# Optimization experiments

Hardware: AMD Instinct MI355X
Metric: run time of the kernel (lower is better)

Reference implementation:

```python
import jax, jax.numpy as jnp
import numpy as np

TEMPERATURE = 0.1
SIGMA = 1.0
NUM_CLASSES = 4
INF = 1e8
EPS = 1e-12


def _l2_normalize(x):
    n = jnp.sqrt(jnp.sum(x * x, axis=-1, keepdims=True))
    return x / jnp.maximum(n, EPS)


def _rbf_kernel(y, gamma):
    # y: [M, P] -> [M, M] exp(-gamma * ||yi - yj||^2)
    sq = jnp.sum(y * y, axis=-1)
    d2 = sq[:, None] + sq[None, :] - 2.0 * (y @ y.T)
    d2 = jnp.maximum(d2, 0.0)
    return jnp.exp(-gamma * d2)


def setup_inputs() -> dict:
    key = jax.random.key(0)
    k1, k2, k3, k4 = jax.random.split(key, 4)
    N, D = 2048, 512
    return {
        "z_i": jax.random.normal(k1, (N, D), dtype=jnp.float32),
        "z_j": jax.random.normal(k2, (N, D), dtype=jnp.float32),
        "labels": jax.random.randint(k3, (N,), 0, NUM_CLASSES, dtype=jnp.int64),
        "z_pos": jax.random.uniform(k4, (N, 1), dtype=jnp.float32),
    }


def reference(z_i, z_j, labels, z_pos):
    N = z_i.shape[0]
    zi = _l2_normalize(z_i)
    zj = _l2_normalize(z_j)

    eye_n = jnp.eye(N, dtype=zi.dtype)
    sim_zii = (zi @ zi.T) / TEMPERATURE - INF * eye_n
    sim_zjj = (zj @ zj.T) / TEMPERATURE - INF * eye_n
    sim_zij = (zi @ zj.T) / TEMPERATURE

    # label agreement mask over the 2N x 2N augmented batch
    labs = jax.nn.one_hot(labels, NUM_CLASSES, dtype=jnp.float32)
    L = jnp.concatenate([labs, labs], axis=0)          # [2N, C]
    eye_2n = jnp.eye(2 * N, dtype=jnp.float32)
    mask = (L @ L.T) * (1.0 - eye_2n)

    # RBF kernel weights over positional labels (detached in original)
    all_pos = jnp.tile(z_pos.reshape(N, -1), (2, 1))   # [2N, P]
    gamma = 1.0 / (2.0 * SIGMA ** 2)
    weights = _rbf_kernel(all_pos, gamma) * (1.0 - eye_2n)

    final_weights = weights * mask
    # NB: torch broadcasting divides column j by rowsum[j]; matrix is symmetric
    final_weights = final_weights / final_weights.sum(axis=1)

    top = jnp.concatenate([sim_zii, sim_zij], axis=1)
    bot = jnp.concatenate([sim_zij.T, sim_zjj], axis=1)
    sim_Z = jnp.concatenate([top, bot], axis=0)        # [2N, 2N]

    log_sim_Z = jax.nn.log_softmax(sim_Z, axis=1)
    loss = (-1.0 / N) * jnp.sum(log_sim_Z * final_weights)
    return loss
```

## Files before the change

kernel.cpp:

```cpp
#include <hip/hip_runtime.h>
#include <hip/hip_bf16.h>

#define D 512
#define INV_T 10.0f
#define INF_VAL 1e8f

#define TILE 256
#define BK 32
#define KSTEPS (D / BK)
#define NGT 16
#define NGB (NGT * NGT)
#define TTB 64
#define NCHUNK 64

typedef short bf16x8 __attribute__((ext_vector_type(8)));
typedef float f32x4 __attribute__((ext_vector_type(4)));

typedef __attribute__((address_space(3))) unsigned int lds_uint;
typedef __attribute__((address_space(1))) unsigned int gbl_uint;

__device__ __forceinline__ void async_copy16(const ushort* gsrc, ushort* ldst) {
  __builtin_amdgcn_global_load_lds((const gbl_uint*)gsrc, (lds_uint*)ldst, 16, 0, 0);
}

__device__ inline float wave_reduce_sum(float v) {
#pragma unroll
  for (int off = 32; off > 0; off >>= 1) v += __shfl_xor(v, off);
  return v;
}

__device__ __forceinline__ ushort f2bf(float x) {
  __hip_bfloat16 h = __float2bfloat16(x);
  return *reinterpret_cast<ushort*>(&h);
}

__global__ __launch_bounds__(256) void k_prep(const float* __restrict__ zi,
                                              const float* __restrict__ zj,
                                              ushort* __restrict__ zb,
                                              const int* __restrict__ labels,
                                              const float* __restrict__ zpos,
                                              float* __restrict__ sinv, int N) {
  int b = blockIdx.x;
  if (b < 1024) {
    int wv = threadIdx.x >> 6, lane = threadIdx.x & 63;
    int row = b * 4 + wv;
    const float* src = (row < N) ? (zi + (size_t)row * D) : (zj + (size_t)(row - N) * D);
    const float4* s4 = reinterpret_cast<const float4*>(src);
    float4 v0 = s4[lane];
    float4 v1 = s4[lane + 64];
    float ss = 0.f;
    ss = fmaf(v0.x, v0.x, ss); ss = fmaf(v0.y, v0.y, ss);
    ss = fmaf(v0.z, v0.z, ss); ss = fmaf(v0.w, v0.w, ss);
    ss = fmaf(v1.x, v1.x, ss); ss = fmaf(v1.y, v1.y, ss);
    ss = fmaf(v1.z, v1.z, ss); ss = fmaf(v1.w, v1.w, ss);
    ss = wave_reduce_sum(ss);
    float sc = 1.0f / fmaxf(sqrtf(ss), 1e-12f);
    ushort4 o0 = {f2bf(v0.x * sc), f2bf(v0.y * sc), f2bf(v0.z * sc), f2bf(v0.w * sc)};
    ushort4 o1 = {f2bf(v1.x * sc), f2bf(v1.y * sc), f2bf(v1.z * sc), f2bf(v1.w * sc)};
    ushort4* dst = reinterpret_cast<ushort4*>(zb + (size_t)row * D);
    dst[lane] = o0;
    dst[lane + 64] = o1;
  } else {
    __shared__ float scratch[4];
    int j = b - 1024;
    int lj = labels[j];
    float pj = zpos[j];
    float s = 0.f;
    for (int i = threadIdx.x; i < N; i += 256) {
      if (labels[i] == lj) {
        float d = zpos[i] - pj;
        s += __expf(-0.5f * d * d);
      }
    }
    s = wave_reduce_sum(s);
    int lane = threadIdx.x & 63, wv = threadIdx.x >> 6;
    if (lane == 0) scratch[wv] = s;
    __syncthreads();
    if (threadIdx.x == 0) {
      float t = scratch[0] + scratch[1] + scratch[2] + scratch[3];
      sinv[j] = 1.0f / (2.0f * t - 1.0f);
    }
  }
}

__global__ __launch_bounds__(512, 2) void k_main(
    const ushort* __restrict__ zb, const int* __restrict__ labels,
    const float* __restrict__ zpos, const float* __restrict__ sinv,
    float* __restrict__ tt,
    float* __restrict__ s_ws, float* __restrict__ c_ws, int N) {
  const int tid = threadIdx.x;
  const int bid = blockIdx.x;
  const int twoN = 2 * N;

  if (bid < TTB) {
    int i = bid * 32 + (tid >> 4);
    int part = tid & 15;
    int li = labels[i];
    float pi = zpos[i];
    int seg = N >> 4;
    float s = 0.f;
    for (int j = part * seg; j < (part + 1) * seg; ++j) {
      if (labels[j] == li) {
        float d = zpos[j] - pi;
        s += __expf(-0.5f * d * d) * sinv[j];
      }
    }
    s += __shfl_xor(s, 1); s += __shfl_xor(s, 2);
    s += __shfl_xor(s, 4); s += __shfl_xor(s, 8);
    if (part == 0) tt[i] = s;
    return;
  }

  __shared__ __align__(16) ushort As[2][TILE * BK];
  __shared__ __align__(16) ushort Bs[2][TILE * BK];

  const int lane = tid & 63;
  const int wv = tid >> 6;
  const int wr = wv >> 2;
  const int wc = wv & 3;
  const int colq = lane & 15;
  const int laneg = lane >> 4;

  int b = bid - TTB;
  int L = (b & 7) * 32 + (b >> 3);
  const int rt = L >> 4;
  const int ct = L & 15;
  const int rowBase = rt * TILE;
  const int colBase = ct * TILE;

  const int srow = lane >> 2;
  const int sslot = (lane & 3) ^ ((lane >> 3) & 3);

  f32x4 acc[8][4] = {};

#define STAGE(buf, kt)                                                        \
  {                                                                           \
    _Pragma("unroll")                                                         \
    for (int q = 0; q < 2; ++q) {                                             \
      int r0 = wv * 32 + q * 16;                                              \
      async_copy16(zb + (size_t)(rowBase + r0 + srow) * D + (kt) * BK +       \
                       sslot * 8,                                             \
                   As[buf] + r0 * BK);                                        \
      async_copy16(zb + (size_t)(colBase + r0 + srow) * D + (kt) * BK +       \
                       sslot * 8,                                             \
                   Bs[buf] + r0 * BK);                                        \
    }                                                                         \
  }

  STAGE(0, 0);
  __syncthreads();

  int cur = 0;
#pragma unroll
  for (int kt = 0; kt < KSTEPS; ++kt) {
    if (kt + 1 < KSTEPS) STAGE(cur ^ 1, kt + 1);

    const char* Ab = reinterpret_cast<const char*>(As[cur]);
    const char* Bb = reinterpret_cast<const char*>(Bs[cur]);
    bf16x8 a[8], bf[4];
#pragma unroll
    for (int rf = 0; rf < 8; ++rf) {
      int r = wr * 128 + rf * 16 + colq;
      a[rf] = *reinterpret_cast<const bf16x8*>(
          Ab + r * 64 + ((laneg ^ ((r >> 1) & 3)) << 4));
    }
#pragma unroll
    for (int cf = 0; cf < 4; ++cf) {
      int c = wc * 64 + cf * 16 + colq;
      bf[cf] = *reinterpret_cast<const bf16x8*>(
          Bb + c * 64 + ((laneg ^ ((c >> 1) & 3)) << 4));
    }
#pragma unroll
    for (int rf = 0; rf < 8; ++rf)
#pragma unroll
      for (int cf = 0; cf < 4; ++cf)
        acc[rf][cf] = __builtin_amdgcn_mfma_f32_16x16x32_bf16(a[rf], bf[cf], acc[rf][cf], 0, 0, 0);

    if (kt + 1 < KSTEPS) {
      __syncthreads();
      cur ^= 1;
    }
  }
#undef STAGE

  const int wRowBase = rowBase + wr * 128;
  const int wColBase = colBase + wc * 64;
  const int rmodBase = (wRowBase >= N) ? wRowBase - N : wRowBase;
  const int cmodBase = (wColBase >= N) ? wColBase - N : wColBase;

  int lc[4]; float pc[4], si[4];
#pragma unroll
  for (int cf = 0; cf < 4; ++cf) {
    int jc = cmodBase + cf * 16 + colq;
    lc[cf] = labels[jc];
    pc[cf] = zpos[jc];
    si[cf] = sinv[jc];
  }
  const int m = ct * 4 + wc;

#pragma unroll
  for (int rf = 0; rf < 8; ++rf) {
    float rpos[4]; int rlab[4];
#pragma unroll
    for (int rg = 0; rg < 4; ++rg) {
      int r = rmodBase + rf * 16 + laneg * 4 + rg;
      rpos[rg] = zpos[r];
      rlab[rg] = labels[r];
    }
    float s_p[4] = {0.f, 0.f, 0.f, 0.f};
    float c_p[4] = {0.f, 0.f, 0.f, 0.f};
#pragma unroll
    for (int cf = 0; cf < 4; ++cf) {
      int col = wColBase + cf * 16 + colq;
#pragma unroll
      for (int rg = 0; rg < 4; ++rg) {
        int row = wRowBase + rf * 16 + laneg * 4 + rg;
        float sim = acc[rf][cf][rg] * INV_T;
        bool dg = (row == col);
        if (dg) sim = -INF_VAL;
        s_p[rg] += __expf(sim - 10.f);
        if (rlab[rg] == lc[cf] && !dg) {
          float d = rpos[rg] - pc[cf];
          c_p[rg] = fmaf(__expf(-0.5f * d * d) * si[cf], sim, c_p[rg]);
        }
      }
    }
#pragma unroll
    for (int rg = 0; rg < 4; ++rg) {
#pragma unroll
      for (int off = 1; off < 16; off <<= 1) {
        s_p[rg] += __shfl_xor(s_p[rg], off);
        c_p[rg] += __shfl_xor(c_p[rg], off);
      }
    }
    if (colq == 0) {
#pragma unroll
      for (int rg = 0; rg < 4; ++rg) {
        int row = wRowBase + rf * 16 + laneg * 4 + rg;
        s_ws[(size_t)m * twoN + row] = s_p[rg];
        c_ws[(size_t)m * twoN + row] = c_p[rg];
      }
    }
  }
}

__global__ __launch_bounds__(256) void k_combine(const float* __restrict__ s_ws,
                                                 const float* __restrict__ c_ws,
                                                 const float* __restrict__ sinv,
                                                 const float* __restrict__ tt,
                                                 float* __restrict__ bsum, int N) {
  __shared__ float sS[4][64], sC[4][64];
  int b = blockIdx.x, t = threadIdx.x;
  int r = t & 63, g = t >> 6;
  int twoN = 2 * N;
  int a = b * 64 + r;
  float s = 0.f, c = 0.f;
  for (int k = 0; k < NCHUNK / 4; ++k) {
    int m = g * (NCHUNK / 4) + k;
    s += s_ws[(size_t)m * twoN + a];
    c += c_ws[(size_t)m * twoN + a];
  }
  sS[g][r] = s;
  sC[g][r] = c;
  __syncthreads();
  if (t < 64) {
    float st = sS[0][t] + sS[1][t] + sS[2][t] + sS[3][t];
    float ct = sC[0][t] + sC[1][t] + sC[2][t] + sC[3][t];
    int aa = b * 64 + t;
    int ir = (aa >= N) ? aa - N : aa;
    float lse = 10.f + logf(st);
    float wsum = 2.f * tt[ir] - sinv[ir];
    float p = ct - wsum * lse;
    p = wave_reduce_sum(p);
    if (t == 0) bsum[b] = p;
  }
}

__global__ __launch_bounds__(64) void k_final(const float* __restrict__ bsum,
                                              float* __restrict__ out, int N) {
  float s = bsum[threadIdx.x];
  s = wave_reduce_sum(s);
  if (threadIdx.x == 0) out[0] = (-1.0f / (float)N) * s;
}

extern "C" void kernel_launch(void* const* d_in, const int* in_sizes, int n_in,
                              void* d_out, int out_size, void* d_ws, size_t ws_size,
                              hipStream_t stream) {
  (void)n_in; (void)out_size; (void)ws_size;
  const float* zi = (const float*)d_in[0];
  const float* zj = (const float*)d_in[1];
  const int* labels = (const int*)d_in[2];
  const float* zpos = (const float*)d_in[3];
  float* out = (float*)d_out;

  const int N = in_sizes[2];
  const int twoN = 2 * N;

  char* wsb = (char*)d_ws;
  ushort* zb = (ushort*)wsb;
  float* sinv = (float*)(wsb + (size_t)twoN * D * 2);
  float* tt = sinv + N;
  float* s_ws = tt + N;
  float* c_ws = s_ws + (size_t)NCHUNK * twoN;
  float* bsum = c_ws + (size_t)NCHUNK * twoN;

  k_prep<<<1024 + 2048, 256, 0, stream>>>(zi, zj, zb, labels, zpos, sinv, N);
  k_main<<<TTB + NGB, 512, 0, stream>>>(zb, labels, zpos, sinv, tt, s_ws, c_ws, N);
  k_combine<<<twoN / 64, 256, 0, stream>>>(s_ws, c_ws, sinv, tt, bsum, N);
  k_final<<<1, 64, 0, stream>>>(bsum, out, N);
}
```

Measured before the change: 70.75 us.

## Shrink GEMM tiles to 128x128 with 256-thread blocks and restructure epilogue

The fused similarity GEMM now uses 128x128 output tiles computed by four waves in 256-thread blocks, instead of 256x256 tiles with 512 threads. That gives 1024 tiles rather than 256, spreading work more evenly across CUs and allowing more resident blocks per CU. The epilogue now keeps all 16 row partials in registers, packs row labels into a bitfield, loads each column's metadata once, and reduces once at the end. The label-weight blocks move to the end of the grid and handle 16 rows each. Smaller tiles reuse each loaded operand less, so L2 and global load traffic rises.

```diff
diff --git a/kernel.cpp b/kernel.cpp
--- a/kernel.cpp
+++ b/kernel.cpp
@@ -5,12 +5,12 @@
 #define INV_T 10.0f
 #define INF_VAL 1e8f
 
-#define TILE 256
+#define BM 128
 #define BK 32
 #define KSTEPS (D / BK)
-#define NGT 16
-#define NGB (NGT * NGT)
-#define TTB 64
+#define NTB 32
+#define NGB (NTB * NTB)
+#define TTBLK 128
 #define NCHUNK 64
 
 typedef short bf16x8 __attribute__((ext_vector_type(8)));
@@ -83,7 +83,7 @@
   }
 }
 
-__global__ __launch_bounds__(512, 2) void k_main(
+__global__ __launch_bounds__(256, 4) void k_gemm(
     const ushort* __restrict__ zb, const int* __restrict__ labels,
     const float* __restrict__ zpos, const float* __restrict__ sinv,
     float* __restrict__ tt,
@@ -92,8 +92,8 @@
   const int bid = blockIdx.x;
   const int twoN = 2 * N;
 
-  if (bid < TTB) {
-    int i = bid * 32 + (tid >> 4);
+  if (bid >= NGB) {
+    int i = (bid - NGB) * 16 + (tid >> 4);
     int part = tid & 15;
     int li = labels[i];
     float pi = zpos[i];
@@ -111,27 +111,26 @@
     return;
   }
 
-  __shared__ __align__(16) ushort As[2][TILE * BK];
-  __shared__ __align__(16) ushort Bs[2][TILE * BK];
+  __shared__ __align__(16) ushort As[2][BM * BK];
+  __shared__ __align__(16) ushort Bs[2][BM * BK];
 
   const int lane = tid & 63;
   const int wv = tid >> 6;
-  const int wr = wv >> 2;
-  const int wc = wv & 3;
+  const int wr = wv >> 1;
+  const int wc = wv & 1;
   const int colq = lane & 15;
   const int laneg = lane >> 4;
 
-  int b = bid - TTB;
-  int L = (b & 7) * 32 + (b >> 3);
-  const int rt = L >> 4;
-  const int ct = L & 15;
-  const int rowBase = rt * TILE;
-  const int colBase = ct * TILE;
+  const int L = (bid & 7) * 128 + (bid >> 3);
+  const int rt = L >> 5;
+  const int ct = L & 31;
+  const int rowBase = rt * BM;
+  const int colBase = ct * BM;
 
   const int srow = lane >> 2;
   const int sslot = (lane & 3) ^ ((lane >> 3) & 3);
 
-  f32x4 acc[8][4] = {};
+  f32x4 acc[4][4] = {};
 
 #define STAGE(buf, kt)                                                        \
   {                                                                           \
@@ -157,24 +156,24 @@
 
     const char* Ab = reinterpret_cast<const char*>(As[cur]);
     const char* Bb = reinterpret_cast<const char*>(Bs[cur]);
-    bf16x8 a[8], bf[4];
-#pragma unroll
-    for (int rf = 0; rf < 8; ++rf) {
-      int r = wr * 128 + rf * 16 + colq;
+    bf16x8 a[4], b[4];
+#pragma unroll
+    for (int rf = 0; rf < 4; ++rf) {
+      int r = wr * 64 + rf * 16 + colq;
       a[rf] = *reinterpret_cast<const bf16x8*>(
           Ab + r * 64 + ((laneg ^ ((r >> 1) & 3)) << 4));
     }
 #pragma unroll
     for (int cf = 0; cf < 4; ++cf) {
       int c = wc * 64 + cf * 16 + colq;
-      bf[cf] = *reinterpret_cast<const bf16x8*>(
+      b[cf] = *reinterpret_cast<const bf16x8*>(
           Bb + c * 64 + ((laneg ^ ((c >> 1) & 3)) << 4));
     }
 #pragma unroll
-    for (int rf = 0; rf < 8; ++rf)
+    for (int rf = 0; rf < 4; ++rf)
 #pragma unroll
       for (int cf = 0; cf < 4; ++cf)
-        acc[rf][cf] = __builtin_amdgcn_mfma_f32_16x16x32_bf16(a[rf], bf[cf], acc[rf][cf], 0, 0, 0);
+        acc[rf][cf] = __builtin_amdgcn_mfma_f32_16x16x32_bf16(a[rf], b[cf], acc[rf][cf], 0, 0, 0);
 
     if (kt + 1 < KSTEPS) {
       __syncthreads();
@@ -183,64 +182,71 @@
   }
 #undef STAGE
 
-  const int wRowBase = rowBase + wr * 128;
+  const int wRowBase = rowBase + wr * 64;
   const int wColBase = colBase + wc * 64;
   const int rmodBase = (wRowBase >= N) ? wRowBase - N : wRowBase;
   const int cmodBase = (wColBase >= N) ? wColBase - N : wColBase;
 
-  int lc[4]; float pc[4], si[4];
+  float rpos[16];
+  unsigned rlab = 0;
+#pragma unroll
+  for (int rf = 0; rf < 4; ++rf)
+#pragma unroll
+    for (int rg = 0; rg < 4; ++rg) {
+      int idx = rf * 4 + rg;
+      int r = rmodBase + rf * 16 + laneg * 4 + rg;
+      rpos[idx] = zpos[r];
+      rlab |= ((unsigned)labels[r] & 3u) << (idx * 2);
+    }
+
+  float s_p[16], c_p[16];
+#pragma unroll
+  for (int i = 0; i < 16; ++i) { s_p[i] = 0.f; c_p[i] = 0.f; }
+
 #pragma unroll
   for (int cf = 0; cf < 4; ++cf) {
     int jc = cmodBase + cf * 16 + colq;
-    lc[cf] = labels[jc];
-    pc[cf] = zpos[jc];
-    si[cf] = sinv[jc];
-  }
-  const int m = ct * 4 + wc;
-
-#pragma unroll
-  for (int rf = 0; rf < 8; ++rf) {
-    float rpos[4]; int rlab[4];
-#pragma unroll
-    for (int rg = 0; rg < 4; ++rg) {
-      int r = rmodBase + rf * 16 + laneg * 4 + rg;
-      rpos[rg] = zpos[r];
-      rlab[rg] = labels[r];
-    }
-    float s_p[4] = {0.f, 0.f, 0.f, 0.f};
-    float c_p[4] = {0.f, 0.f, 0.f, 0.f};
-#pragma unroll
-    for (int cf = 0; cf < 4; ++cf) {
-      int col = wColBase + cf * 16 + colq;
+    int lc = labels[jc];
+    float pc = zpos[jc];
+    float si = sinv[jc];
+    int col = wColBase + cf * 16 + colq;
+#pragma unroll
+    for (int rf = 0; rf < 4; ++rf)
 #pragma unroll
       for (int rg = 0; rg < 4; ++rg) {
+        int idx = rf * 4 + rg;
         int row = wRowBase + rf * 16 + laneg * 4 + rg;
         float sim = acc[rf][cf][rg] * INV_T;
         bool dg = (row == col);
         if (dg) sim = -INF_VAL;
-        s_p[rg] += __expf(sim - 10.f);
-        if (rlab[rg] == lc[cf] && !dg) {
-          float d = rpos[rg] - pc[cf];
-          c_p[rg] = fmaf(__expf(-0.5f * d * d) * si[cf], sim, c_p[rg]);
+        s_p[idx] += __expf(sim - 10.f);
+        int lr = (int)((rlab >> (idx * 2)) & 3u);
+        if (lr == lc && !dg) {
+          float d = rpos[idx] - pc;
+          c_p[idx] = fmaf(__expf(-0.5f * d * d) * si, sim, c_p[idx]);
         }
       }
-    }
-#pragma unroll
-    for (int rg = 0; rg < 4; ++rg) {
-#pragma unroll
-      for (int off = 1; off < 16; off <<= 1) {
-        s_p[rg] += __shfl_xor(s_p[rg], off);
-        c_p[rg] += __shfl_xor(c_p[rg], off);
+  }
+
+#pragma unroll
+  for (int idx = 0; idx < 16; ++idx) {
+#pragma unroll
+    for (int off = 1; off < 16; off <<= 1) {
+      s_p[idx] += __shfl_xor(s_p[idx], off);
+      c_p[idx] += __shfl_xor(c_p[idx], off);
+    }
+  }
+  if (colq == 0) {
+    int m = ct * 2 + wc;
+#pragma unroll
+    for (int rf = 0; rf < 4; ++rf)
+#pragma unroll
+      for (int rg = 0; rg < 4; ++rg) {
+        int idx = rf * 4 + rg;
+        int row = wRowBase + rf * 16 + laneg * 4 + rg;
+        s_ws[(size_t)m * twoN + row] = s_p[idx];
+        c_ws[(size_t)m * twoN + row] = c_p[idx];
       }
-    }
-    if (colq == 0) {
-#pragma unroll
-      for (int rg = 0; rg < 4; ++rg) {
-        int row = wRowBase + rf * 16 + laneg * 4 + rg;
-        s_ws[(size_t)m * twoN + row] = s_p[rg];
-        c_ws[(size_t)m * twoN + row] = c_p[rg];
-      }
-    }
   }
 }
 
@@ -305,7 +311,7 @@
   float* bsum = c_ws + (size_t)NCHUNK * twoN;
 
   k_prep<<<1024 + 2048, 256, 0, stream>>>(zi, zj, zb, labels, zpos, sinv, N);
-  k_main<<<TTB + NGB, 512, 0, stream>>>(zb, labels, zpos, sinv, tt, s_ws, c_ws, N);
+  k_gemm<<<NGB + TTBLK, 256, 0, stream>>>(zb, labels, zpos, sinv, tt, s_ws, c_ws, N);
   k_combine<<<twoN / 64, 256, 0, stream>>>(s_ws, c_ws, sinv, tt, bsum, N);
   k_final<<<1, 64, 0, stream>>>(bsum, out, N);
 }
```

Result: slower. 84.87 us (+20.0%).
